# Kernel optimization log

Hardware: AMD Instinct MI355X
Metric: run time of the kernel (lower is better)

Reference implementation:

```python
import jax, jax.numpy as jnp
import numpy as np

B, T, C = 4, 2048, 1024
H = 16
D = C // H  # head_dim = 64
SCALE = D ** -0.5


def setup_inputs() -> dict:
    key = jax.random.key(0)
    ks = jax.random.split(key, 5)
    x = jax.random.normal(ks[0], (B, T, C), dtype=jnp.float32)
    w_qkv = jax.random.normal(ks[1], (3 * C, C), dtype=jnp.float32) * (C ** -0.5)
    b_qkv = jnp.zeros((3 * C,), dtype=jnp.float32)
    w_proj = jax.random.normal(ks[2], (C, C), dtype=jnp.float32) * (C ** -0.5)
    b_proj = jnp.zeros((C,), dtype=jnp.float32)
    return {"x": x, "w_qkv": w_qkv, "b_qkv": b_qkv, "w_proj": w_proj, "b_proj": b_proj}


def reference(x, w_qkv, b_qkv, w_proj, b_proj):
    b, t, c = x.shape
    # fused qkv projection (torch Linear: x @ W.T + b)
    qkv = x @ w_qkv.T + b_qkv                      # [B, T, 3C]
    q, k, v = jnp.split(qkv, 3, axis=2)
    # [B, T, C] -> [B, H, T, D]
    q = q.reshape(b, t, H, D).transpose(0, 2, 1, 3)
    k = k.reshape(b, t, H, D).transpose(0, 2, 1, 3)
    v = v.reshape(b, t, H, D).transpose(0, 2, 1, 3)
    att = jnp.einsum('bhqd,bhkd->bhqk', q, k) * SCALE
    causal = jnp.tril(jnp.ones((t, t), dtype=bool))  # True = keep
    att = jnp.where(causal, att, -jnp.inf)
    att = jax.nn.softmax(att, axis=-1)
    out = jnp.einsum('bhqk,bhkd->bhqd', att, v)
    out = out.transpose(0, 2, 1, 3).reshape(b, t, c)
    return out @ w_proj.T + b_proj
```

## Files before the change

### kernel.cpp

```cpp
#include <hip/hip_runtime.h>

typedef unsigned short u16;
typedef __attribute__((ext_vector_type(8))) short short8;
typedef __attribute__((ext_vector_type(4))) float f32x4;
typedef __attribute__((ext_vector_type(16))) float f32x16;
typedef __attribute__((ext_vector_type(2))) unsigned uint2v;
typedef __attribute__((ext_vector_type(4))) unsigned u32x4;

#define AS1 __attribute__((address_space(1)))
#define AS3 __attribute__((address_space(3)))

constexpr int Bn = 4, Tn = 2048, Cn = 1024, Hn = 16, Dn = 64;
constexpr float SCL_LOG2E = 0.125f * 1.44269504088896f;

__device__ __forceinline__ u16 f2bf(float f) {
  union { float f; unsigned u; } v; v.f = f;
  unsigned r = v.u + 0x7FFFu + ((v.u >> 16) & 1u);
  return (u16)(r >> 16);
}

__device__ __forceinline__ unsigned cvtpk_bf16(float a, float b) {
  unsigned r;
  asm("v_cvt_pk_bf16_f32 %0, %1, %2" : "=v"(r) : "v"(a), "v"(b));
  return r;
}

__global__ void cast_f32_to_bf16(const float* __restrict__ in, u16* __restrict__ out, int n4) {
  int i = blockIdx.x * 256 + threadIdx.x;
  if (i >= n4) return;
  float4 v = ((const float4*)in)[i];
  ushort4 o;
  o.x = f2bf(v.x); o.y = f2bf(v.y); o.z = f2bf(v.z); o.w = f2bf(v.w);
  ((ushort4*)out)[i] = o;
}

__device__ __forceinline__ void store_out(u16* p, float v) { *p = f2bf(v); }
__device__ __forceinline__ void store_out(float* p, float v) { *p = v; }

template <typename OT>
__global__ __launch_bounds__(256) void gemm_nt(
    const u16* __restrict__ A, const u16* __restrict__ Bm,
    const float* __restrict__ bias, OT* __restrict__ C,
    int M, int N, int K, int qcols, float qscale)
{
  __shared__ u16 As[128 * 32];
  __shared__ u16 Bs[128 * 32];
  const int tid = threadIdx.x;
  const int lane = tid & 63;
  const int wave = tid >> 6;
  const int m0 = blockIdx.y * 128;
  const int n0 = blockIdx.x * 128;
  const int wr = (wave >> 1) * 64;
  const int wc = (wave & 1) * 64;
  const int l15 = lane & 15;
  const int lg = lane >> 4;

  f32x4 acc[4][4] = {};

  for (int kt = 0; kt < K; kt += 32) {
#pragma unroll
    for (int it = 0; it < 2; ++it) {
      int c = it * 256 + tid;
      int row = c >> 2;
      int cc = c & 3;
      int cs = cc ^ ((row >> 1) & 3);
      const u16* ga = A + (m0 + row) * K + kt + cs * 8;
      __builtin_amdgcn_global_load_lds((const AS1 void*)ga, (AS3 void*)(As + c * 8), 16, 0, 0);
      const u16* gb = Bm + (n0 + row) * K + kt + cs * 8;
      __builtin_amdgcn_global_load_lds((const AS1 void*)gb, (AS3 void*)(Bs + c * 8), 16, 0, 0);
    }
    __syncthreads();

    short8 af[4], bfr[4];
#pragma unroll
    for (int i = 0; i < 4; ++i) {
      int rowa = wr + i * 16 + l15;
      int csa = lg ^ ((rowa >> 1) & 3);
      af[i] = *(const short8*)(As + (rowa * 32 + csa * 8));
      int rowb = wc + i * 16 + l15;
      int csb = lg ^ ((rowb >> 1) & 3);
      bfr[i] = *(const short8*)(Bs + (rowb * 32 + csb * 8));
    }
#pragma unroll
    for (int i = 0; i < 4; ++i)
#pragma unroll
      for (int j = 0; j < 4; ++j)
        acc[i][j] = __builtin_amdgcn_mfma_f32_16x16x32_bf16(af[i], bfr[j], acc[i][j], 0, 0, 0);
    __syncthreads();
  }

#pragma unroll
  for (int i = 0; i < 4; ++i) {
    int rowg = m0 + wr + i * 16 + lg * 4;
#pragma unroll
    for (int j = 0; j < 4; ++j) {
      int colg = n0 + wc + j * 16 + l15;
      float sc = (colg < qcols) ? qscale : 1.0f;
      float bv = bias[colg];
#pragma unroll
      for (int r = 0; r < 4; ++r)
        store_out(C + (size_t)(rowg + r) * N + colg, (acc[i][j][r] + bv) * sc);
    }
  }
}

__global__ __launch_bounds__(256) void transpose_v(
    const u16* __restrict__ qkv, u16* __restrict__ vt)
{
  __shared__ u16 tile[64][72];
  const int bh = blockIdx.x >> 5;
  const int tt = blockIdx.x & 31;
  const int b = bh >> 4;
  const int h = bh & 15;
  const int tid = threadIdx.x;
  const int trow = tid >> 2;
  const int dseg = tid & 3;

  const u16* src = qkv + (size_t)(b * Tn + tt * 64 + trow) * (3 * Cn) + 2 * Cn + h * Dn + dseg * 16;
  short8 v0 = *(const short8*)src;
  short8 v1 = *(const short8*)(src + 8);
#pragma unroll
  for (int e = 0; e < 8; ++e) {
    tile[dseg * 16 + e][trow] = (u16)v0[e];
    tile[dseg * 16 + 8 + e][trow] = (u16)v1[e];
  }
  __syncthreads();

  const int drow = tid >> 2;
  const int tseg = tid & 3;
  u16* dst = vt + (size_t)(bh * Dn + drow) * Tn + tt * 64 + tseg * 16;
  *(short8*)dst = *(const short8*)&tile[drow][tseg * 16];
  *(short8*)(dst + 8) = *(const short8*)&tile[drow][tseg * 16 + 8];
}

__global__ __launch_bounds__(256) void attn_kernel(
    const u16* __restrict__ qkv, const u16* __restrict__ vt, u16* __restrict__ att)
{
  __shared__ u16 Ks[2][64 * 64];
  __shared__ u16 Vs[2][64 * 64];
  const int tid = threadIdx.x;
  const int lane = tid & 63;
  const int w = tid >> 6;
  const int l31 = lane & 31;
  const int hi = lane >> 5;

  const int blk = blockIdx.x;
  const int qt = (Tn / 128 - 1) - (blk >> 6);
  const int bh = blk & 63;
  const int b = bh >> 4;
  const int h = bh & 15;
  const int q0w = qt * 128 + w * 32;
  const int rowbase = b * Tn;
  const int koff = Cn + h * Dn;
  const size_t vbase = (size_t)bh * Dn * Tn;
  const int nt = 2 * qt + 2;
  const int ntw = 2 * qt + 1 + (w >> 1);

  short8 qf[4];
  {
    const u16* qp = qkv + (size_t)(rowbase + q0w + l31) * (3 * Cn) + h * Dn + hi * 8;
#pragma unroll
    for (int sub = 0; sub < 4; ++sub) qf[sub] = *(const short8*)(qp + sub * 16);
  }

  float m_r = -1e30f, l_r = 0.f;
  f32x16 oacc[2] = {};

#define STAGE(buf, t_)                                                            \
  {                                                                               \
    const int kt_ = (t_) * 64;                                                    \
    _Pragma("unroll")                                                             \
    for (int it = 0; it < 2; ++it) {                                              \
      int c = it * 256 + tid;                                                     \
      int row = c >> 3;                                                           \
      int cs = (c & 7) ^ (row & 7);                                               \
      const u16* gk = qkv + (size_t)(rowbase + kt_ + row) * (3 * Cn) + koff + cs * 8; \
      __builtin_amdgcn_global_load_lds((const AS1 void*)gk, (AS3 void*)(&Ks[buf][c * 8]), 16, 0, 0); \
      const u16* gv = vt + vbase + (size_t)row * Tn + kt_ + cs * 8;               \
      __builtin_amdgcn_global_load_lds((const AS1 void*)gv, (AS3 void*)(&Vs[buf][c * 8]), 16, 0, 0); \
    }                                                                             \
  }

  STAGE(0, 0);
  __syncthreads();

  for (int t = 0; t < nt; ++t) {
    const int cur = t & 1;
    if (t + 1 < nt) STAGE(cur ^ 1, t + 1);
    if (t < ntw) {
      const int kt = t * 64;
      const u16* Kb = Ks[cur];
      const u16* Vb = Vs[cur];

      f32x16 s0 = {}, s1 = {};
#pragma unroll
      for (int sub = 0; sub < 4; ++sub) {
        const int ch = sub * 2 + hi;
        const int r0 = l31;
        short8 kf0 = *(const short8*)(Kb + r0 * 64 + ((ch ^ (r0 & 7)) << 3));
        s0 = __builtin_amdgcn_mfma_f32_32x32x16_bf16(kf0, qf[sub], s0, 0, 0, 0);
        const int r1 = 32 + l31;
        short8 kf1 = *(const short8*)(Kb + r1 * 64 + ((ch ^ (r1 & 7)) << 3));
        s1 = __builtin_amdgcn_mfma_f32_32x32x16_bf16(kf1, qf[sub], s1, 0, 0, 0);
      }

      if (kt + 63 > q0w) {
        const int qa = q0w + l31;
#pragma unroll
        for (int r = 0; r < 16; ++r) {
          const int k0 = kt + ((r & 3) + 8 * (r >> 2)) + 4 * hi;
          if (k0 > qa) s0[r] = -1e30f;
          if (k0 + 32 > qa) s1[r] = -1e30f;
        }
      }

      float mx = s0[0];
#pragma unroll
      for (int r = 1; r < 16; ++r) mx = fmaxf(mx, s0[r]);
#pragma unroll
      for (int r = 0; r < 16; ++r) mx = fmaxf(mx, s1[r]);
      mx = fmaxf(mx, __shfl_xor(mx, 32));

      if (__any(mx > m_r + 8.f)) {
        const float mnew = fmaxf(m_r, mx);
        const float a = __builtin_amdgcn_exp2f(m_r - mnew);
        m_r = mnew;
        l_r *= a;
#pragma unroll
        for (int r = 0; r < 16; ++r) { oacc[0][r] *= a; oacc[1][r] *= a; }
      }

      float ps = 0.f;
#pragma unroll
      for (int r = 0; r < 16; ++r) {
        s0[r] = __builtin_amdgcn_exp2f(s0[r] - m_r); ps += s0[r];
        s1[r] = __builtin_amdgcn_exp2f(s1[r] - m_r); ps += s1[r];
      }
      ps += __shfl_xor(ps, 32);
      l_r += ps;

      short8 pfr[4];
#pragma unroll
      for (int ks = 0; ks < 4; ++ks) {
        const f32x16& sv = (ks < 2) ? s0 : s1;
        const int base = (ks & 1) * 8;
        unsigned a0 = cvtpk_bf16(sv[base + 0], sv[base + 1]);
        unsigned a1 = cvtpk_bf16(sv[base + 2], sv[base + 3]);
        unsigned b0 = cvtpk_bf16(sv[base + 4], sv[base + 5]);
        unsigned b1 = cvtpk_bf16(sv[base + 6], sv[base + 7]);
        uint2v s_0 = __builtin_amdgcn_permlane32_swap(a0, b0, false, false);
        uint2v s_1 = __builtin_amdgcn_permlane32_swap(a1, b1, false, false);
        union { u32x4 u; short8 s; } cvt;
        cvt.u = (u32x4){s_0.x, s_1.x, s_0.y, s_1.y};
        pfr[ks] = cvt.s;
      }

#pragma unroll
      for (int j = 0; j < 2; ++j) {
        const int rv = j * 32 + l31;
        const int rsw = (rv & 7) << 3;
#pragma unroll
        for (int ks = 0; ks < 4; ++ks) {
          short8 vf = *(const short8*)(Vb + rv * 64 + (((ks * 2 + hi) << 3) ^ rsw));
          oacc[j] = __builtin_amdgcn_mfma_f32_32x32x16_bf16(vf, pfr[ks], oacc[j], 0, 0, 0);
        }
      }
    }
    __syncthreads();
  }

  {
    const float inv = __builtin_amdgcn_rcpf(l_r);
    u16* orow = att + (size_t)(rowbase + q0w + l31) * Cn + h * Dn + hi * 4;
#pragma unroll
    for (int j = 0; j < 2; ++j)
#pragma unroll
      for (int g = 0; g < 4; ++g) {
        ushort4 o;
#pragma unroll
        for (int c = 0; c < 4; ++c) o[c] = f2bf(oacc[j][g * 4 + c] * inv);
        *(ushort4*)(orow + j * 32 + g * 8) = o;
      }
  }
#undef STAGE
}

extern "C" void kernel_launch(void* const* d_in, const int* in_sizes, int n_in,
                              void* d_out, int out_size, void* d_ws, size_t ws_size,
                              hipStream_t stream) {
  const float* x      = (const float*)d_in[0];
  const float* w_qkv  = (const float*)d_in[1];
  const float* b_qkv  = (const float*)d_in[2];
  const float* w_proj = (const float*)d_in[3];
  const float* b_proj = (const float*)d_in[4];
  float* out = (float*)d_out;

  char* ws = (char*)d_ws;
  u16* x_bf     = (u16*)(ws);
  u16* wqkv_bf  = (u16*)(ws + 16777216);
  u16* wproj_bf = (u16*)(ws + 16777216 + 6291456);
  u16* qkv      = (u16*)(ws + 25165824);
  u16* att      = (u16*)(ws + 75497472);
  u16* vt       = x_bf;

  const int M = Bn * Tn;

  cast_f32_to_bf16<<<(M * Cn / 4 + 255) / 256, 256, 0, stream>>>(x, x_bf, M * Cn / 4);
  cast_f32_to_bf16<<<(3 * Cn * Cn / 4 + 255) / 256, 256, 0, stream>>>(w_qkv, wqkv_bf, 3 * Cn * Cn / 4);
  cast_f32_to_bf16<<<(Cn * Cn / 4 + 255) / 256, 256, 0, stream>>>(w_proj, wproj_bf, Cn * Cn / 4);

  gemm_nt<u16><<<dim3(3 * Cn / 128, M / 128), 256, 0, stream>>>(
      x_bf, wqkv_bf, b_qkv, qkv, M, 3 * Cn, Cn, Cn, SCL_LOG2E);

  transpose_v<<<Bn * Hn * (Tn / 64), 256, 0, stream>>>(qkv, vt);

  attn_kernel<<<Bn * Hn * (Tn / 128), 256, 0, stream>>>(qkv, vt, att);

  gemm_nt<float><<<dim3(Cn / 128, M / 128), 256, 0, stream>>>(
      att, wproj_bf, b_proj, out, M, Cn, Cn, 0, 1.0f);
}
```

Before: 185.4 us.

## Replace GEMM with 8-wave double-buffered pipelined kernel using larger tiles

Replaces the simple 128x128, 4-wave, single-buffered GEMM with an 8-wave kernel that uses 256x256 (QKV) or 128x256 (proj) tiles, K-step 64, and double-buffered LDS. Global-to-LDS loads for the next tile are interleaved between quarter-tile MFMA blocks, with manual waitcnt, barriers, setprio, and an XCD-aware block remap. The goal is to hide memory latency and raise MFMA utilization in both projection GEMMs. In exchange the LDS and register footprint grows, which lowers occupancy, and the hand-written barrier and waitcnt schedule is fragile.

```diff
diff --git a/kernel.cpp b/kernel.cpp
--- a/kernel.cpp
+++ b/kernel.cpp
@@ -37,66 +37,133 @@
 __device__ __forceinline__ void store_out(u16* p, float v) { *p = f2bf(v); }
 __device__ __forceinline__ void store_out(float* p, float v) { *p = v; }
 
-template <typename OT>
-__global__ __launch_bounds__(256) void gemm_nt(
+template <int BM, int BN, typename OT>
+__global__ __launch_bounds__(512) void gemm8(
     const u16* __restrict__ A, const u16* __restrict__ Bm,
     const float* __restrict__ bias, OT* __restrict__ C,
-    int M, int N, int K, int qcols, float qscale)
+    int M, int N, int K, int nbn, int qcols, float qscale)
 {
-  __shared__ u16 As[128 * 32];
-  __shared__ u16 Bs[128 * 32];
+  constexpr int NHA = BM / 128, NHB = BN / 128, NH = NHA + NHB;
+  constexpr int MR = BM / 32;
+  constexpr int NR = BN / 64;
+  __shared__ u16 As[2][BM * 64];
+  __shared__ u16 Bs[2][BN * 64];
+
   const int tid = threadIdx.x;
   const int lane = tid & 63;
-  const int wave = tid >> 6;
-  const int m0 = blockIdx.y * 128;
-  const int n0 = blockIdx.x * 128;
-  const int wr = (wave >> 1) * 64;
-  const int wc = (wave & 1) * 64;
-  const int l15 = lane & 15;
-  const int lg = lane >> 4;
-
-  f32x4 acc[4][4] = {};
-
-  for (int kt = 0; kt < K; kt += 32) {
+  const int w = tid >> 6;
+  const int wm = w >> 2, wn = w & 3;
+  const int l15 = lane & 15, lg = lane >> 4;
+
+  const int nwg = gridDim.x;
+  const int wg = (blockIdx.x & 7) * (nwg >> 3) + (blockIdx.x >> 3);
+  const int m0 = (wg / nbn) * BM;
+  const int n0 = (wg % nbn) * BN;
+  const int NT = K >> 6;
+
+  const int wrow = wm * (BM / 2);
+  const int wcol = wn * (BN / 4);
+
+  f32x4 acc[MR][NR] = {};
+
+  auto stage_half = [&](int tt, int h) {
+    if (tt >= NT) return;
+    const int bu = tt & 1;
 #pragma unroll
     for (int it = 0; it < 2; ++it) {
-      int c = it * 256 + tid;
-      int row = c >> 2;
-      int cc = c & 3;
-      int cs = cc ^ ((row >> 1) & 3);
-      const u16* ga = A + (m0 + row) * K + kt + cs * 8;
-      __builtin_amdgcn_global_load_lds((const AS1 void*)ga, (AS3 void*)(As + c * 8), 16, 0, 0);
-      const u16* gb = Bm + (n0 + row) * K + kt + cs * 8;
-      __builtin_amdgcn_global_load_lds((const AS1 void*)gb, (AS3 void*)(Bs + c * 8), 16, 0, 0);
+      const int c = it * 512 + tid;
+      const int row = c >> 3;
+      const int cs = (c & 7) ^ (row & 7);
+      if (h < NHA) {
+        const u16* g = A + (size_t)(m0 + h * 128 + row) * K + tt * 64 + cs * 8;
+        __builtin_amdgcn_global_load_lds((const AS1 void*)g,
+            (AS3 void*)(&As[bu][(h * 128 + row) * 64 + (c & 7) * 8]), 16, 0, 0);
+      } else {
+        const int rb = (h - NHA) * 128 + row;
+        const u16* g = Bm + (size_t)(n0 + rb) * K + tt * 64 + cs * 8;
+        __builtin_amdgcn_global_load_lds((const AS1 void*)g,
+            (AS3 void*)(&Bs[bu][rb * 64 + (c & 7) * 8]), 16, 0, 0);
+      }
     }
-    __syncthreads();
-
-    short8 af[4], bfr[4];
-#pragma unroll
-    for (int i = 0; i < 4; ++i) {
-      int rowa = wr + i * 16 + l15;
-      int csa = lg ^ ((rowa >> 1) & 3);
-      af[i] = *(const short8*)(As + (rowa * 32 + csa * 8));
-      int rowb = wc + i * 16 + l15;
-      int csb = lg ^ ((rowb >> 1) & 3);
-      bfr[i] = *(const short8*)(Bs + (rowb * 32 + csb * 8));
+  };
+
+  auto readA = [&](int bu, int mh, short8 (*a)[2]) {
+#pragma unroll
+    for (int i = 0; i < MR / 2; ++i)
+#pragma unroll
+      for (int ks = 0; ks < 2; ++ks) {
+        const int ra = wrow + (mh * (MR / 2) + i) * 16 + l15;
+        a[i][ks] = *(const short8*)(&As[bu][ra * 64 + (((ks * 4 + lg) ^ (ra & 7)) << 3)]);
+      }
+  };
+  auto readB = [&](int bu, int nh, short8 (*b)[2]) {
+#pragma unroll
+    for (int j = 0; j < NR / 2; ++j)
+#pragma unroll
+      for (int ks = 0; ks < 2; ++ks) {
+        const int rb = wcol + (nh * (NR / 2) + j) * 16 + l15;
+        b[j][ks] = *(const short8*)(&Bs[bu][rb * 64 + (((ks * 4 + lg) ^ (rb & 7)) << 3)]);
+      }
+  };
+  auto mmaq = [&](int mh, int nh, short8 (*a)[2], short8 (*b)[2]) {
+    __builtin_amdgcn_s_setprio(1);
+#pragma unroll
+    for (int i = 0; i < MR / 2; ++i)
+#pragma unroll
+      for (int j = 0; j < NR / 2; ++j)
+#pragma unroll
+        for (int ks = 0; ks < 2; ++ks)
+          acc[mh * (MR / 2) + i][nh * (NR / 2) + j] =
+              __builtin_amdgcn_mfma_f32_16x16x32_bf16(
+                  a[i][ks], b[j][ks], acc[mh * (MR / 2) + i][nh * (NR / 2) + j], 0, 0, 0);
+    __builtin_amdgcn_s_setprio(0);
+  };
+
+#pragma unroll
+  for (int h = 0; h < NH; ++h) stage_half(0, h);
+  stage_half(1, 0);
+  asm volatile("s_waitcnt vmcnt(2)" ::: "memory");
+  __builtin_amdgcn_sched_barrier(0);
+  __builtin_amdgcn_s_barrier();
+
+  for (int t = 0; t < NT; ++t) {
+    const int bu = t & 1;
+    short8 a0[MR / 2][2], a1[MR / 2][2], b0[NR / 2][2], b1[NR / 2][2];
+    readA(bu, 0, a0);
+    readB(bu, 0, b0);
+    stage_half(t + 1, 1);
+    __builtin_amdgcn_s_barrier();
+    mmaq(0, 0, a0, b0);
+    __builtin_amdgcn_s_barrier();
+    readB(bu, 1, b1);
+    stage_half(t + 1, 2);
+    __builtin_amdgcn_s_barrier();
+    mmaq(0, 1, a0, b1);
+    __builtin_amdgcn_s_barrier();
+    readA(bu, 1, a1);
+    if constexpr (NH > 3) stage_half(t + 1, 3);
+    __builtin_amdgcn_s_barrier();
+    mmaq(1, 1, a1, b1);
+    __builtin_amdgcn_s_barrier();
+    stage_half(t + 2, 0);
+    __builtin_amdgcn_s_barrier();
+    mmaq(1, 0, a1, b0);
+    if (t < NT - 1) {
+      if (t + 2 < NT) asm volatile("s_waitcnt vmcnt(2)" ::: "memory");
+      else            asm volatile("s_waitcnt vmcnt(0)" ::: "memory");
+      __builtin_amdgcn_sched_barrier(0);
     }
-#pragma unroll
-    for (int i = 0; i < 4; ++i)
-#pragma unroll
-      for (int j = 0; j < 4; ++j)
-        acc[i][j] = __builtin_amdgcn_mfma_f32_16x16x32_bf16(af[i], bfr[j], acc[i][j], 0, 0, 0);
-    __syncthreads();
-  }
-
-#pragma unroll
-  for (int i = 0; i < 4; ++i) {
-    int rowg = m0 + wr + i * 16 + lg * 4;
-#pragma unroll
-    for (int j = 0; j < 4; ++j) {
-      int colg = n0 + wc + j * 16 + l15;
-      float sc = (colg < qcols) ? qscale : 1.0f;
-      float bv = bias[colg];
+    __builtin_amdgcn_s_barrier();
+  }
+
+#pragma unroll
+  for (int i = 0; i < MR; ++i) {
+    const int rowg = m0 + wrow + i * 16 + lg * 4;
+#pragma unroll
+    for (int j = 0; j < NR; ++j) {
+      const int colg = n0 + wcol + j * 16 + l15;
+      const float sc = (colg < qcols) ? qscale : 1.0f;
+      const float bv = bias[colg];
 #pragma unroll
       for (int r = 0; r < 4; ++r)
         store_out(C + (size_t)(rowg + r) * N + colg, (acc[i][j][r] + bv) * sc);
@@ -309,13 +376,13 @@
   cast_f32_to_bf16<<<(3 * Cn * Cn / 4 + 255) / 256, 256, 0, stream>>>(w_qkv, wqkv_bf, 3 * Cn * Cn / 4);
   cast_f32_to_bf16<<<(Cn * Cn / 4 + 255) / 256, 256, 0, stream>>>(w_proj, wproj_bf, Cn * Cn / 4);
 
-  gemm_nt<u16><<<dim3(3 * Cn / 128, M / 128), 256, 0, stream>>>(
-      x_bf, wqkv_bf, b_qkv, qkv, M, 3 * Cn, Cn, Cn, SCL_LOG2E);
+  gemm8<256, 256, u16><<<384, 512, 0, stream>>>(
+      x_bf, wqkv_bf, b_qkv, qkv, M, 3 * Cn, Cn, 12, Cn, SCL_LOG2E);
 
   transpose_v<<<Bn * Hn * (Tn / 64), 256, 0, stream>>>(qkv, vt);
 
   attn_kernel<<<Bn * Hn * (Tn / 128), 256, 0, stream>>>(qkv, vt, att);
 
-  gemm_nt<float><<<dim3(Cn / 128, M / 128), 256, 0, stream>>>(
-      att, wproj_bf, b_proj, out, M, Cn, Cn, 0, 1.0f);
-}
+  gemm8<128, 256, float><<<256, 512, 0, stream>>>(
+      att, wproj_bf, b_proj, out, M, Cn, Cn, 4, 0, 1.0f);
+}
```

New measurement: 177.7 us. -4.1%, faster.
